# Performance work log

Measured on AMD Instinct MI355X. Metric: run time of the kernel, lower is better.

Reference implementation:

```python
import jax, jax.numpy as jnp
import numpy as np

QUERY_DIM = 1024
CONTEXT_DIM = 1024
HEADS = 8
DIM_HEAD = 64
INNER = HEADS * DIM_HEAD  # 512
B, NQ, NC = 2, 1024, 1024


def setup_inputs() -> dict:
    key = jax.random.key(0)
    ks = jax.random.split(key, 9)
    s_in_q = 1.0 / np.sqrt(QUERY_DIM)
    s_in_c = 1.0 / np.sqrt(CONTEXT_DIM)
    s_in_o = 1.0 / np.sqrt(INNER)
    return {
        "x": jax.random.normal(ks[0], (B, NQ, QUERY_DIM), dtype=jnp.float32),
        "context": jax.random.normal(ks[1], (B, NC, CONTEXT_DIM), dtype=jnp.float32),
        "mask": jnp.ones((B, NQ + NC), dtype=bool),
        # weights stored as [in, out] (transpose of torch Linear.weight)
        "Wq": jax.random.normal(ks[2], (QUERY_DIM, INNER), dtype=jnp.float32) * s_in_q,
        "Wk": jax.random.normal(ks[3], (CONTEXT_DIM, INNER), dtype=jnp.float32) * s_in_c,
        "Wv": jax.random.normal(ks[4], (CONTEXT_DIM, INNER), dtype=jnp.float32) * s_in_c,
        "Wv_self": jax.random.normal(ks[5], (QUERY_DIM, INNER), dtype=jnp.float32) * s_in_q,
        "Wo": jax.random.normal(ks[6], (INNER, QUERY_DIM), dtype=jnp.float32) * s_in_o,
        "bo": jnp.zeros((QUERY_DIM,), dtype=jnp.float32),
    }


def reference(x, context, mask, Wq, Wk, Wv, Wv_self, Wo, bo):
    h, d = HEADS, DIM_HEAD
    scale = d ** (-0.5)
    b, nq, _ = x.shape

    q = x @ Wq                                   # [b, nq, inner]
    k = context @ Wk                             # [b, nc, inner]
    v_cross = context @ Wv                       # [b, nc, inner]
    v_self = jax.lax.stop_gradient(x @ Wv_self)  # detached in original

    qc = jnp.concatenate([q, k], axis=1)         # [b, n, inner], n = nq+nc
    kc = qc                                      # k = q.clone()
    v = jnp.concatenate([v_self, v_cross], axis=1)

    def split_heads(t):
        bb, n, _ = t.shape
        return t.reshape(bb, n, h, d).transpose(0, 2, 1, 3)  # [b, h, n, d]

    qh, kh, vh = split_heads(qc), split_heads(kc), split_heads(v)

    sim = jnp.einsum('bhid,bhjd->bhij', qh, kh) * scale      # [b, h, n, n]
    neg = -jnp.finfo(sim.dtype).max
    sim = jnp.where(mask[:, None, None, :], sim, neg)
    attn = jax.nn.softmax(sim, axis=-1)
    out = jnp.einsum('bhij,bhjd->bhid', attn, vh)            # [b, h, n, d]

    gated = out[:, :, :nq, :]                                # first nq queries
    gated = gated.transpose(0, 2, 1, 3).reshape(b, nq, h * d)
    return gated @ Wo + bo
```

## Files before the change

kernel.cpp:

```cpp
#include <hip/hip_runtime.h>

typedef __bf16 bf16;
typedef __bf16 bf16x8 __attribute__((ext_vector_type(8)));
typedef __bf16 bf16x4v __attribute__((ext_vector_type(4)));
typedef float f32x4 __attribute__((ext_vector_type(4)));
typedef short short4v __attribute__((ext_vector_type(4)));

__device__ __forceinline__ f32x4 mfma16(bf16x8 a, bf16x8 b, f32x4 c) {
  return __builtin_amdgcn_mfma_f32_16x16x32_bf16(a, b, c, 0, 0, 0);
}

__device__ __forceinline__ f32x4 mfma16k16(bf16x4v a, bf16x4v b, f32x4 c) {
#if __has_builtin(__builtin_amdgcn_mfma_f32_16x16x16_bf16)
  return __builtin_amdgcn_mfma_f32_16x16x16_bf16(a, b, c, 0, 0, 0);
#else
  return __builtin_amdgcn_mfma_f32_16x16x16bf16_1k(
      __builtin_bit_cast(short4v, a), __builtin_bit_cast(short4v, b), c, 0, 0, 0);
#endif
}

__device__ __forceinline__ void load16_lds(const void* g, void* l) {
  __builtin_amdgcn_global_load_lds(
      (const __attribute__((address_space(1))) void*)(unsigned long long)g,
      (__attribute__((address_space(3))) void*)(unsigned long long)l, 16, 0, 0);
}

__global__ __launch_bounds__(256) void prep(
    const float4* __restrict__ x, const float4* __restrict__ c,
    bf16x4v* __restrict__ xb, bf16x4v* __restrict__ cb,
    const float* __restrict__ Wq, const float* __restrict__ Wk,
    const float* __restrict__ Wv, const float* __restrict__ Wvs,
    const float* __restrict__ Wo,
    bf16* __restrict__ WqT, bf16* __restrict__ WkT, bf16* __restrict__ WvT,
    bf16* __restrict__ WsT, bf16* __restrict__ WoT) {
  int bid = blockIdx.x;
  if (bid < 4096) {
    int i = bid * 256 + threadIdx.x;
    const float4* s; bf16x4v* d; int j;
    if (i < 524288) { s = x; d = xb; j = i; }
    else            { s = c; d = cb; j = i - 524288; }
    float4 f = s[j];
    bf16x4v o;
    o[0] = (bf16)f.x; o[1] = (bf16)f.y; o[2] = (bf16)f.z; o[3] = (bf16)f.w;
    d[j] = o;
    return;
  }
  __shared__ float tile[32][33];
  int bid2 = bid - 4096;
  int z = bid2 >> 10, rem = bid2 & 1023;
  const float* src; bf16* dst; int K, N;
  switch (z) {
    case 0: src = Wq;  dst = WqT; K = 1024; N = 512;  break;
    case 1: src = Wk;  dst = WkT; K = 1024; N = 512;  break;
    case 2: src = Wv;  dst = WvT; K = 1024; N = 512;  break;
    case 3: src = Wvs; dst = WsT; K = 1024; N = 512;  break;
    default: src = Wo; dst = WoT; K = 512;  N = 1024; break;
  }
  int n0 = (rem & 31) * 32, k0 = (rem >> 5) * 32;
  if (n0 >= N || k0 >= K) return;
  int tx = threadIdx.x & 31, ty = threadIdx.x >> 5;
#pragma unroll
  for (int i = 0; i < 32; i += 8)
    tile[ty + i][tx] = src[(size_t)(k0 + ty + i) * N + n0 + tx];
  __syncthreads();
  int n = threadIdx.x >> 3, k4 = (threadIdx.x & 7) * 4;
  bf16x4v o4;
#pragma unroll
  for (int e = 0; e < 4; e++) o4[e] = (bf16)tile[k4 + e][n];
  *(bf16x4v*)&dst[(size_t)(n0 + n) * K + k0 + k4] = o4;
}

__global__ __launch_bounds__(256) void qkv_gemm(
    const bf16* __restrict__ xb, const bf16* __restrict__ cb,
    const bf16* __restrict__ WqT, const bf16* __restrict__ WkT,
    const bf16* __restrict__ WvT, const bf16* __restrict__ WsT,
    bf16* __restrict__ qc, bf16* __restrict__ vT) {
  __shared__ __align__(16) bf16 As[128 * 64];
  __shared__ __align__(16) bf16 Bs[64 * 64];
  int m0 = blockIdx.y * 128, n0 = blockIdx.x * 64;
  int b = m0 >> 11, r0 = m0 & 2047;
  bool rowHalf = r0 < 1024;
  const bf16* Abase = rowHalf ? (xb + (size_t)(b * 1024 + r0) * 1024)
                              : (cb + (size_t)(b * 1024 + (r0 - 1024)) * 1024);
  bool colHalf = n0 < 512;
  const bf16* WT = colHalf ? (rowHalf ? WqT : WkT) : (rowHalf ? WsT : WvT);
  int nW = colHalf ? n0 : n0 - 512;
  const bf16* Bbase = WT + (size_t)nW * 1024;

  int tid = threadIdx.x;
  int lane = tid & 63, w = tid >> 6;
  int low = lane & 15, quad = lane >> 4;
  f32x4 acc[4][2] = {};

  for (int kk = 0; kk < 1024; kk += 64) {
#pragma unroll
    for (int t = 0; t < 4; t++) {
      int p = t * 256 + tid;
      int row = p >> 3, c8 = (p & 7) ^ (row & 7);
      load16_lds(Abase + (size_t)row * 1024 + kk + c8 * 8, As + (t * 256 + w * 64) * 8);
    }
#pragma unroll
    for (int t = 0; t < 2; t++) {
      int p = t * 256 + tid;
      int row = p >> 3, c8 = (p & 7) ^ (row & 7);
      load16_lds(Bbase + (size_t)row * 1024 + kk + c8 * 8, Bs + (t * 256 + w * 64) * 8);
    }
    __syncthreads();
#pragma unroll
    for (int kk2 = 0; kk2 < 2; kk2++) {
      bf16x8 af[4], bfr[2];
      int mb = (w >> 1) * 64 + low;
#pragma unroll
      for (int mi = 0; mi < 4; mi++) {
        int row = mb + mi * 16;
        af[mi] = *(const bf16x8*)&As[row * 64 + ((kk2 * 4 + quad) ^ (row & 7)) * 8];
      }
#pragma unroll
      for (int ni = 0; ni < 2; ni++) {
        int row = (w & 1) * 32 + ni * 16 + low;
        bfr[ni] = *(const bf16x8*)&Bs[row * 64 + ((kk2 * 4 + quad) ^ (row & 7)) * 8];
      }
#pragma unroll
      for (int mi = 0; mi < 4; mi++)
#pragma unroll
        for (int ni = 0; ni < 2; ni++) acc[mi][ni] = mfma16(af[mi], bfr[ni], acc[mi][ni]);
    }
    __syncthreads();
  }

#pragma unroll
  for (int mi = 0; mi < 4; mi++) {
    int rowg = m0 + (w >> 1) * 64 + mi * 16 + quad * 4;
#pragma unroll
    for (int ni = 0; ni < 2; ni++) {
      int col = n0 + (w & 1) * 32 + ni * 16 + low;
      if (col < 512) {
#pragma unroll
        for (int r = 0; r < 4; r++)
          qc[(size_t)(rowg + r) * 512 + col] = (bf16)acc[mi][ni][r];
      } else {
        int d = col - 512;
        int bb = rowg >> 11, key = rowg & 2047;
        bf16x4v pk;
#pragma unroll
        for (int r = 0; r < 4; r++) pk[r] = (bf16)acc[mi][ni][r];
        *(bf16x4v*)&vT[((size_t)(bb * 512 + d)) * 2048 + key] = pk;
      }
    }
  }
}

__global__ __launch_bounds__(256) void attn_part(const bf16* __restrict__ qc,
                                                 const bf16* __restrict__ vT,
                                                 bf16* __restrict__ Opart,
                                                 float* __restrict__ lpart) {
  __shared__ __align__(16) bf16 Ks[64 * 64];
  __shared__ __align__(16) bf16 Vs[64 * 64];
  int bh = blockIdx.y, b = bh >> 3, h = bh & 7;
  int q0 = blockIdx.x * 128;
  int ch = blockIdx.z;
  int tid = threadIdx.x, lane = tid & 63, w = tid >> 6;
  int low = lane & 15, quad = lane >> 4;
  const float SC = 0.125f * 1.44269504f;

  const bf16* Qrow = qc + ((size_t)(b * 2048) + q0 + w * 32 + low) * 512 + h * 64;
  bf16x8 qf[2][2];
#pragma unroll
  for (int g = 0; g < 2; g++) {
    qf[g][0] = *(const bf16x8*)(Qrow + (size_t)g * 16 * 512 + quad * 8);
    qf[g][1] = *(const bf16x8*)(Qrow + (size_t)g * 16 * 512 + 32 + quad * 8);
  }

  f32x4 accT[2][4] = {};
  float l_lane[2] = {0.f, 0.f};

  const bf16* Kg = qc + (size_t)(b * 2048) * 512 + h * 64;
  const bf16* Vg = vT + (size_t)(b * 512 + h * 64) * 2048;

  for (int k0 = ch * 512; k0 < ch * 512 + 512; k0 += 64) {
    __syncthreads();
#pragma unroll
    for (int t = 0; t < 2; t++) {
      int p = t * 256 + tid;
      int r = p >> 3, c8 = (p & 7) ^ (r & 7);
      load16_lds(Kg + (size_t)(k0 + r) * 512 + c8 * 8, Ks + (t * 256 + w * 64) * 8);
      load16_lds(Vg + (size_t)r * 2048 + k0 + c8 * 8, Vs + (t * 256 + w * 64) * 8);
    }
    __syncthreads();

    bf16x4v pk[2][4];
#pragma unroll
    for (int kt = 0; kt < 4; kt++) {
      int row = kt * 16 + low, sw = row & 7;
      bf16x8 ka0 = *(const bf16x8*)&Ks[row * 64 + (quad ^ sw) * 8];
      bf16x8 ka1 = *(const bf16x8*)&Ks[row * 64 + ((4 + quad) ^ sw) * 8];
#pragma unroll
      for (int g = 0; g < 2; g++) {
        f32x4 s = {0.f, 0.f, 0.f, 0.f};
        s = mfma16(ka0, qf[g][0], s);
        s = mfma16(ka1, qf[g][1], s);
        float p0 = exp2f(s[0] * SC), p1 = exp2f(s[1] * SC);
        float p2 = exp2f(s[2] * SC), p3 = exp2f(s[3] * SC);
        l_lane[g] += (p0 + p1) + (p2 + p3);
        bf16x4v v;
        v[0] = (bf16)p0; v[1] = (bf16)p1; v[2] = (bf16)p2; v[3] = (bf16)p3;
        pk[g][kt] = v;
      }
    }

#pragma unroll
    for (int dt = 0; dt < 4; dt++) {
      int row = dt * 16 + low, sw = row & 7;
#pragma unroll
      for (int kt = 0; kt < 4; kt++) {
        int c8 = kt * 2 + (quad >> 1);
        bf16x4v va =
            *(const bf16x4v*)&Vs[row * 64 + ((c8 ^ sw)) * 8 + (quad & 1) * 4];
#pragma unroll
        for (int g = 0; g < 2; g++)
          accT[g][dt] = mfma16k16(va, pk[g][kt], accT[g][dt]);
      }
    }
  }

#pragma unroll
  for (int g = 0; g < 2; g++) {
    l_lane[g] += __shfl_xor(l_lane[g], 16, 64);
    l_lane[g] += __shfl_xor(l_lane[g], 32, 64);
    int q = q0 + w * 32 + g * 16 + low;
    if (quad == 0) lpart[((size_t)bh * 1024 + q) * 4 + ch] = l_lane[g];
    bf16* Od = Opart + (((size_t)bh * 1024 + q) * 4 + ch) * 64;
#pragma unroll
    for (int dt = 0; dt < 4; dt++) {
      bf16x4v o;
#pragma unroll
      for (int e = 0; e < 4; e++) o[e] = (bf16)accT[g][dt][e];
      *(bf16x4v*)(Od + dt * 16 + quad * 4) = o;
    }
  }
}

__global__ __launch_bounds__(256) void attn_comb(const bf16* __restrict__ Opart,
                                                 const float* __restrict__ lpart,
                                                 bf16* __restrict__ gated) {
  int bh = blockIdx.y, b = bh >> 3, h = bh & 7;
  int q = blockIdx.x * 64 + (threadIdx.x >> 2);
  int dbase = (threadIdx.x & 3) * 16;
  const float* lp = lpart + ((size_t)bh * 1024 + q) * 4;
  float inv = 1.f / (lp[0] + lp[1] + lp[2] + lp[3]);
  const bf16* Ob = Opart + ((size_t)bh * 1024 + q) * 256;
  bf16* og = gated + ((size_t)(b * 1024) + q) * 512 + h * 64 + dbase;
#pragma unroll
  for (int s = 0; s < 2; s++) {
    float acc[8] = {};
#pragma unroll
    for (int c = 0; c < 4; c++) {
      bf16x8 v = *(const bf16x8*)(Ob + c * 64 + dbase + s * 8);
#pragma unroll
      for (int e = 0; e < 8; e++) acc[e] += (float)v[e];
    }
    bf16x8 o;
#pragma unroll
    for (int e = 0; e < 8; e++) o[e] = (bf16)(acc[e] * inv);
    *(bf16x8*)(og + s * 8) = o;
  }
}

__global__ __launch_bounds__(256) void out_gemm(const bf16* __restrict__ gated,
                                                const bf16* __restrict__ WoT,
                                                const float* __restrict__ bo,
                                                float* __restrict__ out) {
  __shared__ __align__(16) bf16 As[64 * 32];
  __shared__ __align__(16) bf16 Bs[64 * 32];
  int m0 = blockIdx.y * 64, n0 = blockIdx.x * 64;
  int tid = threadIdx.x, lane = tid & 63, w = tid >> 6;
  int low = lane & 15, quad = lane >> 4;
  const bf16* Ab = gated + (size_t)m0 * 512;
  const bf16* Bb = WoT + (size_t)n0 * 512;
  f32x4 acc[2][2] = {};

  for (int kk = 0; kk < 512; kk += 32) {
    int row = tid >> 2, k8 = (tid & 3) * 8;
    load16_lds(Ab + (size_t)row * 512 + kk + k8, As + w * 512);
    load16_lds(Bb + (size_t)row * 512 + kk + k8, Bs + w * 512);
    __syncthreads();
    bf16x8 af[2], bfr[2];
#pragma unroll
    for (int mi = 0; mi < 2; mi++)
      af[mi] = *(const bf16x8*)&As[((w >> 1) * 32 + mi * 16 + low) * 32 + quad * 8];
#pragma unroll
    for (int ni = 0; ni < 2; ni++)
      bfr[ni] = *(const bf16x8*)&Bs[((w & 1) * 32 + ni * 16 + low) * 32 + quad * 8];
#pragma unroll
    for (int mi = 0; mi < 2; mi++)
#pragma unroll
      for (int ni = 0; ni < 2; ni++) acc[mi][ni] = mfma16(af[mi], bfr[ni], acc[mi][ni]);
    __syncthreads();
  }

#pragma unroll
  for (int mi = 0; mi < 2; mi++) {
    int rowg = m0 + (w >> 1) * 32 + mi * 16 + quad * 4;
#pragma unroll
    for (int ni = 0; ni < 2; ni++) {
      int col = n0 + (w & 1) * 32 + ni * 16 + low;
      float bias = bo[col];
#pragma unroll
      for (int r = 0; r < 4; r++)
        out[(size_t)(rowg + r) * 1024 + col] = acc[mi][ni][r] + bias;
    }
  }
}

extern "C" void kernel_launch(void* const* d_in, const int* in_sizes, int n_in,
                              void* d_out, int out_size, void* d_ws, size_t ws_size,
                              hipStream_t stream) {
  const float* x   = (const float*)d_in[0];
  const float* ctx = (const float*)d_in[1];
  const float* Wq  = (const float*)d_in[3];
  const float* Wk  = (const float*)d_in[4];
  const float* Wv  = (const float*)d_in[5];
  const float* Wvs = (const float*)d_in[6];
  const float* Wo  = (const float*)d_in[7];
  const float* bo  = (const float*)d_in[8];
  float* out = (float*)d_out;

  bf16* xb  = (bf16*)d_ws;
  bf16* cb  = xb + 2097152;
  bf16* WqT = cb + 2097152;
  bf16* WkT = WqT + 524288;
  bf16* WvT = WkT + 524288;
  bf16* WsT = WvT + 524288;
  bf16* WoT = WsT + 524288;
  bf16* qcb = WoT + 524288;
  bf16* vTb = qcb + 2097152;
  bf16* gb  = vTb + 2097152;
  bf16* Opart = gb + 1048576;
  float* lb   = (float*)(Opart + 4194304);

  prep<<<9216, 256, 0, stream>>>((const float4*)x, (const float4*)ctx,
                                 (bf16x4v*)xb, (bf16x4v*)cb,
                                 Wq, Wk, Wv, Wvs, Wo, WqT, WkT, WvT, WsT, WoT);
  qkv_gemm<<<dim3(16, 32), 256, 0, stream>>>(xb, cb, WqT, WkT, WvT, WsT, qcb, vTb);
  attn_part<<<dim3(8, 16, 4), 256, 0, stream>>>(qcb, vTb, Opart, lb);
  attn_comb<<<dim3(16, 16), 256, 0, stream>>>(Opart, lb, gb);
  out_gemm<<<dim3(16, 32), 256, 0, stream>>>(gb, WoT, bo, out);
}
```

Before: 138.1 us.

## Fuse split-KV attention combine into output projection GEMM A-tile load

Removes the separate attn_comb kernel and the gated intermediate buffer. out_gemm now reads the four partial attention outputs directly, sums them, normalizes by precomputed inverse row sums held in shared memory, and writes the bf16 A tile to LDS. This saves a launch and an intermediate write/read, but each N-block redundantly re-reads and reduces the 4x larger partials, and the A load becomes synchronous instead of an async global-to-LDS copy.

```diff
diff --git a/kernel.cpp b/kernel.cpp
--- a/kernel.cpp
+++ b/kernel.cpp
@@ -240,49 +240,51 @@
   }
 }
 
-__global__ __launch_bounds__(256) void attn_comb(const bf16* __restrict__ Opart,
-                                                 const float* __restrict__ lpart,
-                                                 bf16* __restrict__ gated) {
-  int bh = blockIdx.y, b = bh >> 3, h = bh & 7;
-  int q = blockIdx.x * 64 + (threadIdx.x >> 2);
-  int dbase = (threadIdx.x & 3) * 16;
-  const float* lp = lpart + ((size_t)bh * 1024 + q) * 4;
-  float inv = 1.f / (lp[0] + lp[1] + lp[2] + lp[3]);
-  const bf16* Ob = Opart + ((size_t)bh * 1024 + q) * 256;
-  bf16* og = gated + ((size_t)(b * 1024) + q) * 512 + h * 64 + dbase;
-#pragma unroll
-  for (int s = 0; s < 2; s++) {
-    float acc[8] = {};
-#pragma unroll
-    for (int c = 0; c < 4; c++) {
-      bf16x8 v = *(const bf16x8*)(Ob + c * 64 + dbase + s * 8);
-#pragma unroll
-      for (int e = 0; e < 8; e++) acc[e] += (float)v[e];
-    }
-    bf16x8 o;
-#pragma unroll
-    for (int e = 0; e < 8; e++) o[e] = (bf16)(acc[e] * inv);
-    *(bf16x8*)(og + s * 8) = o;
-  }
-}
-
-__global__ __launch_bounds__(256) void out_gemm(const bf16* __restrict__ gated,
+__global__ __launch_bounds__(256) void out_gemm(const bf16* __restrict__ Opart,
+                                                const float* __restrict__ lpart,
                                                 const bf16* __restrict__ WoT,
                                                 const float* __restrict__ bo,
                                                 float* __restrict__ out) {
   __shared__ __align__(16) bf16 As[64 * 32];
   __shared__ __align__(16) bf16 Bs[64 * 32];
+  __shared__ float sInv[8 * 64];
   int m0 = blockIdx.y * 64, n0 = blockIdx.x * 64;
   int tid = threadIdx.x, lane = tid & 63, w = tid >> 6;
   int low = lane & 15, quad = lane >> 4;
-  const bf16* Ab = gated + (size_t)m0 * 512;
+  int b = m0 >> 10, qloc = m0 & 1023, b8 = b * 8;
   const bf16* Bb = WoT + (size_t)n0 * 512;
   f32x4 acc[2][2] = {};
 
+#pragma unroll
+  for (int t = 0; t < 2; t++) {
+    int idx = t * 256 + tid;
+    int h = idx >> 6, qr = idx & 63;
+    f32x4 lp = *(const f32x4*)(lpart + ((size_t)(b8 + h) * 1024 + qloc + qr) * 4);
+    sInv[idx] = 1.f / (lp[0] + lp[1] + lp[2] + lp[3]);
+  }
+
+  int qrow = tid >> 2, dsub = (tid & 3) * 8;
   for (int kk = 0; kk < 512; kk += 32) {
-    int row = tid >> 2, k8 = (tid & 3) * 8;
-    load16_lds(Ab + (size_t)row * 512 + kk + k8, As + w * 512);
-    load16_lds(Bb + (size_t)row * 512 + kk + k8, Bs + w * 512);
+    int h = kk >> 6, d0 = kk & 63;
+    const bf16* Ob =
+        Opart + (((size_t)(b8 + h) * 1024 + qloc + qrow) * 4) * 64 + d0 + dsub;
+    __syncthreads();
+    float a[8] = {};
+#pragma unroll
+    for (int c = 0; c < 4; c++) {
+      bf16x8 v = *(const bf16x8*)(Ob + c * 64);
+#pragma unroll
+      for (int e = 0; e < 8; e++) a[e] += (float)v[e];
+    }
+    float inv = sInv[h * 64 + qrow];
+    bf16x8 av;
+#pragma unroll
+    for (int e = 0; e < 8; e++) av[e] = (bf16)(a[e] * inv);
+    *(bf16x8*)&As[qrow * 32 + dsub] = av;
+    {
+      int row = tid >> 2, k8 = (tid & 3) * 8;
+      load16_lds(Bb + (size_t)row * 512 + kk + k8, Bs + w * 512);
+    }
     __syncthreads();
     bf16x8 af[2], bfr[2];
 #pragma unroll
@@ -295,7 +297,6 @@
     for (int mi = 0; mi < 2; mi++)
 #pragma unroll
       for (int ni = 0; ni < 2; ni++) acc[mi][ni] = mfma16(af[mi], bfr[ni], acc[mi][ni]);
-    __syncthreads();
   }
 
 #pragma unroll
@@ -334,8 +335,7 @@
   bf16* WoT = WsT + 524288;
   bf16* qcb = WoT + 524288;
   bf16* vTb = qcb + 2097152;
-  bf16* gb  = vTb + 2097152;
-  bf16* Opart = gb + 1048576;
+  bf16* Opart = vTb + 2097152;
   float* lb   = (float*)(Opart + 4194304);
 
   prep<<<9216, 256, 0, stream>>>((const float4*)x, (const float4*)ctx,
@@ -343,6 +343,5 @@
                                  Wq, Wk, Wv, Wvs, Wo, WqT, WkT, WvT, WsT, WoT);
   qkv_gemm<<<dim3(16, 32), 256, 0, stream>>>(xb, cb, WqT, WkT, WvT, WsT, qcb, vTb);
   attn_part<<<dim3(8, 16, 4), 256, 0, stream>>>(qcb, vTb, Opart, lb);
-  attn_comb<<<dim3(16, 16), 256, 0, stream>>>(Opart, lb, gb);
-  out_gemm<<<dim3(16, 32), 256, 0, stream>>>(gb, WoT, bo, out);
-}
+  out_gemm<<<dim3(16, 32), 256, 0, stream>>>(Opart, lb, WoT, bo, out);
+}
```

New measurement: 143.0 us. +3.5%, slower.
